# Performance work log

Hardware: AMD Instinct MI355X
Metric: run time of the kernel (lower is better)

Reference implementation:

```python
import jax, jax.numpy as jnp
import numpy as np

V = 100000   # nodes
E = 1600000  # edges (avg degree 16)
LN = 64      # feat_dim
S = 8        # stat_dim
T = 4        # recurrence steps
MU = 0.9
N_EDGE_TYPES = 10


def _uniform_linear(kw, kb, fan_out, fan_in):
    # torch nn.Linear default init: U(-1/sqrt(fan_in), 1/sqrt(fan_in))
    lim = 1.0 / np.sqrt(fan_in)
    W = jax.random.uniform(kw, (fan_out, fan_in), jnp.float32, -lim, lim)
    b = jax.random.uniform(kb, (fan_out,), jnp.float32, -lim, lim)
    return W, b


def setup_inputs() -> dict:
    key = jax.random.key(0)
    ks = jax.random.split(key, 12)
    feat_Matrix = jax.random.normal(ks[0], (V, LN), jnp.float32)
    X_Node = jax.random.randint(ks[1], (E,), 1, V + 1, dtype=jnp.int64)   # 1-indexed
    X_Neis = jax.random.randint(ks[2], (E,), 1, V + 1, dtype=jnp.int64)   # 1-indexed
    edge_type_index = jax.random.randint(ks[3], (E,), 1, N_EDGE_TYPES + 1, dtype=jnp.int32)
    dg_list = jax.random.randint(ks[4], (E,), 1, 65).astype(jnp.float32)  # degrees >= 1
    H_init = jax.random.uniform(ks[5], (V, S), jnp.float32)  # torch.rand init of state
    W_xi, b_xi = _uniform_linear(ks[6], ks[7], S * S, 2 * LN + N_EDGE_TYPES)
    W_rou, b_rou = _uniform_linear(ks[8], ks[9], S, LN)
    W1, b1 = _uniform_linear(ks[10], ks[11], 1, S)
    return {
        "feat_Matrix": feat_Matrix, "X_Node": X_Node, "X_Neis": X_Neis,
        "edge_type_index": edge_type_index, "dg_list": dg_list, "H_init": H_init,
        "W_xi": W_xi, "b_xi": b_xi, "W_rou": W_rou, "b_rou": b_rou,
        "W1": W1, "b1": b1,
    }


def reference(feat_Matrix, X_Node, X_Neis, edge_type_index, dg_list, H_init,
              W_xi, b_xi, W_rou, b_rou, W1, b1):
    src = X_Node - 1           # 0-indexed source nodes
    dst = X_Neis - 1           # 0-indexed neighbor nodes (for embedding gather)
    node_emb = feat_Matrix[src]            # [E, LN]
    neis_emb = feat_Matrix[dst]            # [E, LN]
    et = jax.nn.one_hot(edge_type_index - 1, N_EDGE_TYPES, dtype=jnp.float32)
    X = jnp.concatenate([node_emb, neis_emb, et], axis=1)  # [E, 2*LN+10]

    # Xi(X): per-edge transition matrices A, constant across steps -> precompute
    A = jnp.tanh(X @ W_xi.T + b_xi).reshape(-1, S, S)
    A = A * (MU / S) / dg_list[:, None, None]              # [E, S, S]
    # Rou(neis_emb): per-edge bias b, constant across steps
    bias = jnp.tanh(neis_emb @ W_rou.T + b_rou)            # [E, S]

    def step(H, _):
        He = H[src]                                        # gather [E, S]
        out = jnp.einsum('eij,ej->ei', A, He) + bias       # per-edge small matmul
        # AggrSum: dense one-hot mask vs RAW 1-indexed X_Neis against range(0,V-1)
        # -> scatter by 1-indexed ids; ids == V fall out of range and are dropped.
        Hn = jax.ops.segment_sum(out, X_Neis, num_segments=V)
        return Hn, None

    H, _ = jax.lax.scan(step, H_init, None, length=T)      # [V, S]

    logits = (H @ W1.T + b1).squeeze(-1)                   # [V]
    attn = jax.nn.softmax(logits)                          # softmax over nodes
    graph_out = jnp.tanh(jnp.sum(H * attn[:, None], axis=0))  # [S]
    return graph_out
```

## Files before the change

### kernel.cpp

```cpp
#include <hip/hip_runtime.h>
#include <hip/hip_bf16.h>

constexpr int V   = 100000;
constexpr int E   = 1600000;
constexpr int NET = 10;
constexpr int KXW = 138;
constexpr int NB  = (V + 255) / 256;
constexpr int GN  = 8;
constexpr float MUS   = 0.1125f;
constexpr float SP    = 0.025f;
constexpr float LOG2E = 1.44269504f;
constexpr float S2L   = 2.0f * SP * LOG2E;
constexpr float AS    = MUS / 127.0f;

typedef __attribute__((ext_vector_type(8))) short short8;
typedef __attribute__((ext_vector_type(4))) float float4v;

__device__ __forceinline__ float fast_tanh(float x) {
    return 1.0f - 2.0f * __builtin_amdgcn_rcpf(__expf(2.0f * x) + 1.0f);
}
__device__ __forceinline__ float bflo(unsigned u) { return __uint_as_float(u << 16); }
__device__ __forceinline__ float bfhi(unsigned u) { return __uint_as_float(u & 0xffff0000u); }
__device__ __forceinline__ short f2bf(float x) {
    union { __hip_bfloat16 b; short s; } u; u.b = __float2bfloat16(x); return u.s;
}

__device__ __forceinline__ float ub0(unsigned u) {
#if __has_builtin(__builtin_amdgcn_cvt_f32_ubyte0)
    return __builtin_amdgcn_cvt_f32_ubyte0(u);
#else
    return (float)(u & 0xff);
#endif
}
__device__ __forceinline__ float ub1(unsigned u) {
#if __has_builtin(__builtin_amdgcn_cvt_f32_ubyte1)
    return __builtin_amdgcn_cvt_f32_ubyte1(u);
#else
    return (float)((u >> 8) & 0xff);
#endif
}
__device__ __forceinline__ float ub2(unsigned u) {
#if __has_builtin(__builtin_amdgcn_cvt_f32_ubyte2)
    return __builtin_amdgcn_cvt_f32_ubyte2(u);
#else
    return (float)((u >> 16) & 0xff);
#endif
}
__device__ __forceinline__ float ub3(unsigned u) {
#if __has_builtin(__builtin_amdgcn_cvt_f32_ubyte3)
    return __builtin_amdgcn_cvt_f32_ubyte3(u);
#else
    return (float)(u >> 24);
#endif
}
__device__ __forceinline__ unsigned pku8(float f, unsigned pos, unsigned old) {
#if __has_builtin(__builtin_amdgcn_cvt_pk_u8_f32)
    return __builtin_amdgcn_cvt_pk_u8_f32(f, pos, old);
#else
    return old | ((unsigned)f << (8 * pos));
#endif
}

__device__ __forceinline__ int dot4(unsigned a, unsigned b, int c) {
#if __has_builtin(__builtin_amdgcn_sdot4)
    return __builtin_amdgcn_sdot4((int)a, (int)b, c, false);
#else
    int r = c;
    r += ((int)(a << 24) >> 24) * ((int)(b << 24) >> 24);
    r += ((int)(a << 16) >> 24) * ((int)(b << 16) >> 24);
    r += ((int)(a <<  8) >> 24) * ((int)(b <<  8) >> 24);
    r += ((int)a >> 24) * ((int)b >> 24);
    return r;
#endif
}

__global__ __launch_bounds__(256) void histg_kernel(
    const int* __restrict__ xneis, int* __restrict__ countg,
    int* __restrict__ rank0)
{
    int e = blockIdx.x * 256 + threadIdx.x;
    if (e >= E) return;
    int g = blockIdx.x & (GN - 1);
    int nr = xneis[e];
    if (nr < V) rank0[e] = atomicAdd(&countg[g * V + nr], 1);
}

__global__ __launch_bounds__(256) void gprefix_kernel(
    const int* __restrict__ countg, int* __restrict__ offg,
    int* __restrict__ cnt)
{
    int v = blockIdx.x * 256 + threadIdx.x;
    if (v >= V) return;
    int run = 0;
    #pragma unroll
    for (int g = 0; g < GN; ++g) {
        offg[g * V + v] = run;
        run += countg[g * V + v];
    }
    cnt[v] = run;
}

__global__ __launch_bounds__(256) void scan_cnt_kernel(
    const int* __restrict__ cnt, int* __restrict__ scanned, int* __restrict__ bsum)
{
    __shared__ int s[256];
    int tid = threadIdx.x;
    int i = blockIdx.x * 256 + tid;
    int c = (i < V) ? cnt[i] : 0;
    s[tid] = c; __syncthreads();
    #pragma unroll
    for (int off = 1; off < 256; off <<= 1) {
        int t = (tid >= off) ? s[tid - off] : 0;
        __syncthreads();
        s[tid] += t;
        __syncthreads();
    }
    if (i < V) scanned[i] = s[tid] - c;
    if (tid == 255) bsum[blockIdx.x] = s[255];
}

__global__ __launch_bounds__(512) void scan_tops_kernel(
    const int* __restrict__ blocksum, int* __restrict__ tops, int* __restrict__ rowptr)
{
    __shared__ int s[512];
    int tid = threadIdx.x;
    int v = (tid < NB) ? blocksum[tid] : 0;
    s[tid] = v; __syncthreads();
    #pragma unroll
    for (int off = 1; off < 512; off <<= 1) {
        int t = (tid >= off) ? s[tid - off] : 0;
        __syncthreads();
        s[tid] += t;
        __syncthreads();
    }
    if (tid < NB) tops[tid] = s[tid] - v;
    if (tid == 511) rowptr[V] = s[511];
}

__global__ __launch_bounds__(256) void add_offsets_kernel(
    const int* __restrict__ scanned, const int* __restrict__ tops, int* __restrict__ rowptr)
{
    int i = blockIdx.x * 256 + threadIdx.x;
    if (i < V) rowptr[i] = scanned[i] + tops[blockIdx.x];
}

__global__ __launch_bounds__(256) void scatter_kernel(
    const int* __restrict__ xnode, const int* __restrict__ xneis,
    const int* __restrict__ etype, const float* __restrict__ dg,
    const int* __restrict__ rowptr, const int* __restrict__ offg,
    const int* __restrict__ rank0, unsigned* __restrict__ pmeta)
{
    int e = blockIdx.x * 256 + threadIdx.x;
    if (e >= E) return;
    int g = blockIdx.x & (GN - 1);
    int nr = xneis[e];
    if (nr < V) {
        int p = rowptr[nr] + offg[g * V + nr] + rank0[e];
        unsigned src = (unsigned)(xnode[e] - 1);
        unsigned et  = (unsigned)(etype[e] - 1);
        unsigned dgi = (unsigned)dg[e] - 1;
        pmeta[p] = src | (et << 17) | (dgi << 21);
    }
}

__global__ __launch_bounds__(256) void bsum_kernel(
    const float* __restrict__ feat, const int* __restrict__ count,
    const float* __restrict__ Wrou, const float* __restrict__ brou,
    const float* __restrict__ Hinit, float* __restrict__ Bsum,
    uint4* __restrict__ Hq0)
{
    __shared__ float Wl[512];
    __shared__ float bl[8];
    int tid = threadIdx.x;
    for (int i = tid; i < 512; i += 256) Wl[i] = Wrou[i];
    if (tid < 8) bl[tid] = brou[tid];
    __syncthreads();

    int v = blockIdx.x * 256 + tid;
    if (v >= V) return;
    int c = count[v];
    float out[8] = {0, 0, 0, 0, 0, 0, 0, 0};
    if (c > 0) {
        const float4* f4 = (const float4*)(feat + (size_t)(v - 1) * 64);
        float acc[8];
        #pragma unroll
        for (int s = 0; s < 8; ++s) acc[s] = bl[s];
        #pragma unroll 4
        for (int k = 0; k < 16; ++k) {
            float4 x = f4[k];
            #pragma unroll
            for (int s = 0; s < 8; ++s) {
                const float* w = &Wl[s * 64 + k * 4];
                acc[s] += x.x * w[0] + x.y * w[1] + x.z * w[2] + x.w * w[3];
            }
        }
        float fc = (float)c;
        #pragma unroll
        for (int s = 0; s < 8; ++s) out[s] = fc * fast_tanh(acc[s]);
    }
    float4* O = (float4*)(Bsum + (size_t)v * 8);
    O[0] = make_float4(out[0], out[1], out[2], out[3]);
    O[1] = make_float4(out[4], out[5], out[6], out[7]);

    const float4* Hh4 = (const float4*)(Hinit + (size_t)v * 8);
    float4 h0 = Hh4[0], h1 = Hh4[1];
    float hv[8] = {h0.x, h0.y, h0.z, h0.w, h1.x, h1.y, h1.z, h1.w};
    float mx = 0.0f;
    #pragma unroll
    for (int i = 0; i < 8; ++i) mx = fmaxf(mx, fabsf(hv[i]));
    float si = (mx > 0.0f) ? 127.0f / mx : 0.0f;
    unsigned bb[8];
    #pragma unroll
    for (int i = 0; i < 8; ++i) bb[i] = (unsigned)((int)rintf(hv[i] * si)) & 0xffu;
    uint4 o;
    o.x = bb[0] | (bb[1] << 8) | (bb[2] << 16) | (bb[3] << 24);
    o.y = bb[4] | (bb[5] << 8) | (bb[6] << 16) | (bb[7] << 24);
    o.z = __float_as_uint(mx * (1.0f / 127.0f));
    o.w = 0;
    Hq0[v] = o;
}

__global__ __launch_bounds__(256) void pq_kernel(
    const float* __restrict__ feat, const float* __restrict__ Wxi,
    unsigned char* __restrict__ P8, ushort* __restrict__ Qb)
{
    const int lane = threadIdx.x & 63, wave = threadIdx.x >> 6;
    const int quad = lane >> 4, l16 = lane & 15;

    short8 bP[4][2], bQ[4][2];
    #pragma unroll
    for (int nt = 0; nt < 4; ++nt) {
        #pragma unroll
        for (int ks = 0; ks < 2; ++ks) {
            const float* wp = Wxi + (size_t)(nt * 16 + l16) * KXW + ks * 32 + quad * 8;
            short8 p, q;
            #pragma unroll
            for (int j = 0; j < 8; ++j) { p[j] = f2bf(wp[j]); q[j] = f2bf(wp[64 + j]); }
            bP[nt][ks] = p; bQ[nt][ks] = q;
        }
    }

    int t = blockIdx.x * 4 + wave;
    if (t >= V / 16) return;
    int v0 = t * 16;

    const float* fp = feat + (size_t)(v0 + l16) * 64 + quad * 8;
    short8 a0, a1;
    #pragma unroll
    for (int j = 0; j < 8; ++j) { a0[j] = f2bf(fp[j]); a1[j] = f2bf(fp[32 + j]); }

    float4v accP[4], accQ[4];
    #pragma unroll
    for (int nt = 0; nt < 4; ++nt) {
        float4v z = {0.f, 0.f, 0.f, 0.f};
        z = __builtin_amdgcn_mfma_f32_16x16x32_bf16(a0, bP[nt][0], z, 0, 0, 0);
        z = __builtin_amdgcn_mfma_f32_16x16x32_bf16(a1, bP[nt][1], z, 0, 0, 0);
        accP[nt] = z;
        float4v w = {0.f, 0.f, 0.f, 0.f};
        w = __builtin_amdgcn_mfma_f32_16x16x32_bf16(a0, bQ[nt][0], w, 0, 0, 0);
        w = __builtin_amdgcn_mfma_f32_16x16x32_bf16(a1, bQ[nt][1], w, 0, 0, 0);
        accQ[nt] = w;
    }

    #pragma unroll
    for (int r = 0; r < 4; ++r) {
        int row = v0 + quad * 4 + r;
        #pragma unroll
        for (int nt = 0; nt < 4; ++nt) {
            int col = nt * 16 + l16;
            int q8 = (int)rintf(accP[nt][r] * (1.0f / SP)) + 128;
            q8 = min(max(q8, 0), 255);
            P8[row * 64 + col] = (unsigned char)q8;
            Qb[row * 64 + col] = (ushort)f2bf(accQ[nt][r]);
        }
    }
}

__global__ __launch_bounds__(256) void amat_kernel(
    const unsigned* __restrict__ pmeta, const int* __restrict__ rowptr,
    const unsigned char* __restrict__ P8, const ushort* __restrict__ Qb,
    const float* __restrict__ Wxi, const float* __restrict__ bxi,
    const uint4* __restrict__ Hq0, const float* __restrict__ Bsum,
    unsigned char* __restrict__ A8, uint4* __restrict__ HqOut)
{
    __shared__ float Wet2[NET * 64];
    __shared__ float scT[64];
    int tid = threadIdx.x;
    for (int i = tid; i < NET * 64; i += 256) {
        int et = i >> 6, n = i & 63;
        Wet2[i] = 2.0f * LOG2E * (Wxi[n * KXW + 128 + et] + bxi[n]);
    }
    if (tid < 64) scT[tid] = 127.0f / (float)(tid + 1);
    __syncthreads();

    int v = blockIdx.x * 4 + (tid >> 6);
    if (v >= V) return;
    int lane = tid & 63;
    int el = lane >> 3, s = lane & 7;

    const int off = rowptr[v];
    const int deg = rowptr[v + 1] - off;

    float q0, q1, q2, q3, q4, q5, q6, q7;
    {
        uint4 qu = *(const uint4*)(Qb + v * 64 + s * 8);
        const float B = 128.0f * SP, C = 2.0f * LOG2E;
        q0 = C * (bflo(qu.x) - B); q1 = C * (bfhi(qu.x) - B);
        q2 = C * (bflo(qu.y) - B); q3 = C * (bfhi(qu.y) - B);
        q4 = C * (bflo(qu.z) - B); q5 = C * (bfhi(qu.z) - B);
        q6 = C * (bflo(qu.w) - B); q7 = C * (bfhi(qu.w) - B);
    }

    float accD = 0.0f;

    for (int base = 0; base < deg; base += 64) {
        unsigned m_mine = 0;
        {
            int i1 = base + lane;
            if (i1 < deg) m_mine = pmeta[off + i1];
        }
        int nb = deg - base;
        for (int k = 0; k * 8 + el < nb && k < 8; ++k) {
            int ib = k * 8 + el;
            int i = base + ib;
            unsigned m = __shfl(m_mine, ib);
            int src = (int)(m & 0x1FFFF);
            int et  = (int)((m >> 17) & 0xF);
            float kk  = scT[m >> 21];
            float m2k = -2.0f * kk;
            float ck  = kk + 128.5f;

            uint2 pu = *(const uint2*)(P8 + src * 64 + s * 8);
            const float4* w4 = (const float4*)(&Wet2[et * 64 + s * 8]);
            float4 wa = w4[0], wb = w4[1];
            uint4 hq = Hq0[src];

            float r0 = __builtin_amdgcn_rcpf(__builtin_amdgcn_exp2f(fmaf(ub0(pu.x), S2L, q0 + wa.x)) + 1.0f);
            float r1 = __builtin_amdgcn_rcpf(__builtin_amdgcn_exp2f(fmaf(ub1(pu.x), S2L, q1 + wa.y)) + 1.0f);
            float r2 = __builtin_amdgcn_rcpf(__builtin_amdgcn_exp2f(fmaf(ub2(pu.x), S2L, q2 + wa.z)) + 1.0f);
            float r3 = __builtin_amdgcn_rcpf(__builtin_amdgcn_exp2f(fmaf(ub3(pu.x), S2L, q3 + wa.w)) + 1.0f);
            float r4 = __builtin_amdgcn_rcpf(__builtin_amdgcn_exp2f(fmaf(ub0(pu.y), S2L, q4 + wb.x)) + 1.0f);
            float r5 = __builtin_amdgcn_rcpf(__builtin_amdgcn_exp2f(fmaf(ub1(pu.y), S2L, q5 + wb.y)) + 1.0f);
            float r6 = __builtin_amdgcn_rcpf(__builtin_amdgcn_exp2f(fmaf(ub2(pu.y), S2L, q6 + wb.z)) + 1.0f);
            float r7 = __builtin_amdgcn_rcpf(__builtin_amdgcn_exp2f(fmaf(ub3(pu.y), S2L, q7 + wb.w)) + 1.0f);

            float qf0 = fmaf(r0, m2k, ck), qf1 = fmaf(r1, m2k, ck);
            float qf2 = fmaf(r2, m2k, ck), qf3 = fmaf(r3, m2k, ck);
            float qf4 = fmaf(r4, m2k, ck), qf5 = fmaf(r5, m2k, ck);
            float qf6 = fmaf(r6, m2k, ck), qf7 = fmaf(r7, m2k, ck);

            uint2 o;
            o.x = pku8(qf3, 3, pku8(qf2, 2, pku8(qf1, 1, pku8(qf0, 0, 0u)))) ^ 0x80808080u;
            o.y = pku8(qf7, 3, pku8(qf6, 2, pku8(qf5, 1, pku8(qf4, 0, 0u)))) ^ 0x80808080u;
            *(uint2*)(A8 + (unsigned)(off + i) * 64u + (unsigned)(s * 8)) = o;

            int dd = dot4(o.x, hq.x, dot4(o.y, hq.y, 0));
            accD = fmaf((float)dd, __uint_as_float(hq.z), accD);
        }
    }
    accD += __shfl_xor(accD, 8);  accD += __shfl_xor(accD, 16); accD += __shfl_xor(accD, 32);
    float h1v = accD * AS + Bsum[v * 8 + s];

    float mx = fabsf(h1v);
    mx = fmaxf(mx, __shfl_xor(mx, 1));
    mx = fmaxf(mx, __shfl_xor(mx, 2));
    mx = fmaxf(mx, __shfl_xor(mx, 4));
    float si = (mx > 0.0f) ? 127.0f / mx : 0.0f;
    unsigned b = (unsigned)((int)rintf(h1v * si)) & 0xffu;
    unsigned b1 = __shfl(b, lane + 1), b2 = __shfl(b, lane + 2), b3 = __shfl(b, lane + 3);
    unsigned b4 = __shfl(b, lane + 4), b5 = __shfl(b, lane + 5);
    unsigned b6 = __shfl(b, lane + 6), b7 = __shfl(b, lane + 7);
    if (lane == 0) {
        uint4 hq;
        hq.x = b  | (b1 << 8) | (b2 << 16) | (b3 << 24);
        hq.y = b4 | (b5 << 8) | (b6 << 16) | (b7 << 24);
        hq.z = __float_as_uint(mx * (1.0f / 127.0f));
        hq.w = 0;
        HqOut[v] = hq;
    }
}

__global__ __launch_bounds__(256) void step_kernel(
    const uint4* __restrict__ HqIn, uint4* __restrict__ HqOut,
    const unsigned* __restrict__ pmeta, const int* __restrict__ rowptr,
    const unsigned char* __restrict__ A8, const float* __restrict__ Bsum,
    const float* __restrict__ W1, const float* __restrict__ b1,
    float* __restrict__ logitsOut, float* __restrict__ HfpOut)
{
    int v = blockIdx.x * 4 + (threadIdx.x >> 6);
    if (v >= V) return;
    int lane = threadIdx.x & 63;
    int el = lane >> 2, q = lane & 3;

    int p0 = rowptr[v], p1 = rowptr[v + 1];

    float accE = 0.0f, accO = 0.0f;
    int p = p0 + el;
    for (; p + 16 < p1; p += 32) {
        int srcA = (int)(pmeta[p] & 0x1FFFFu);
        int srcB = (int)(pmeta[p + 16] & 0x1FFFFu);
        uint4 auA = *(const uint4*)(A8 + (unsigned)p * 64u + (unsigned)(q * 16));
        uint4 auB = *(const uint4*)(A8 + (unsigned)(p + 16) * 64u + (unsigned)(q * 16));
        uint4 hqA = HqIn[srcA];
        uint4 hqB = HqIn[srcB];

        int dEA = dot4(auA.x, hqA.x, dot4(auA.y, hqA.y, 0));
        int dOA = dot4(auA.z, hqA.x, dot4(auA.w, hqA.y, 0));
        float sA = __uint_as_float(hqA.z);
        accE = fmaf((float)dEA, sA, accE);
        accO = fmaf((float)dOA, sA, accO);

        int dEB = dot4(auB.x, hqB.x, dot4(auB.y, hqB.y, 0));
        int dOB = dot4(auB.z, hqB.x, dot4(auB.w, hqB.y, 0));
        float sB = __uint_as_float(hqB.z);
        accE = fmaf((float)dEB, sB, accE);
        accO = fmaf((float)dOB, sB, accO);
    }
    if (p < p1) {
        int src = (int)(pmeta[p] & 0x1FFFFu);
        uint4 au = *(const uint4*)(A8 + (unsigned)p * 64u + (unsigned)(q * 16));
        uint4 hq = HqIn[src];
        int dE = dot4(au.x, hq.x, dot4(au.y, hq.y, 0));
        int dO = dot4(au.z, hq.x, dot4(au.w, hq.y, 0));
        float sc = __uint_as_float(hq.z);
        accE = fmaf((float)dE, sc, accE);
        accO = fmaf((float)dO, sc, accO);
    }
    accE += __shfl_xor(accE, 4);  accE += __shfl_xor(accE, 8);
    accE += __shfl_xor(accE, 16); accE += __shfl_xor(accE, 32);
    accO += __shfl_xor(accO, 4);  accO += __shfl_xor(accO, 8);
    accO += __shfl_xor(accO, 16); accO += __shfl_xor(accO, 32);

    float hE = accE * AS + Bsum[v * 8 + q * 2];
    float hO = accO * AS + Bsum[v * 8 + q * 2 + 1];

    float mx = fmaxf(fabsf(hE), fabsf(hO));
    mx = fmaxf(mx, __shfl_xor(mx, 1));
    mx = fmaxf(mx, __shfl_xor(mx, 2));
    float si = (mx > 0.0f) ? 127.0f / mx : 0.0f;
    unsigned qE = (unsigned)((int)rintf(hE * si)) & 0xffu;
    unsigned qO = (unsigned)((int)rintf(hO * si)) & 0xffu;
    unsigned hw  = qE | (qO << 8);
    unsigned hw1 = __shfl(hw, lane + 1), hw2 = __shfl(hw, lane + 2);
    unsigned hw3 = __shfl(hw, lane + 3);
    if (lane == 0) {
        uint4 o;
        o.x = hw  | (hw1 << 16);
        o.y = hw2 | (hw3 << 16);
        o.z = __float_as_uint(mx * (1.0f / 127.0f));
        o.w = 0;
        HqOut[v] = o;
    }
    if (HfpOut != nullptr && el == 0)
        *(float2*)(HfpOut + v * 8 + q * 2) = make_float2(hE, hO);
    if (logitsOut != nullptr) {
        float t = hE * W1[q * 2] + hO * W1[q * 2 + 1];
        t += __shfl_xor(t, 1); t += __shfl_xor(t, 2);
        if (lane == 0) logitsOut[v] = t + b1[0];
    }
}

__global__ __launch_bounds__(256) void reduce_max_kernel(
    const float* __restrict__ logits, float* __restrict__ partial)
{
    float m = -INFINITY;
    for (int v = blockIdx.x * 256 + threadIdx.x; v < V; v += 256 * 256)
        m = fmaxf(m, logits[v]);
    #pragma unroll
    for (int o = 32; o > 0; o >>= 1) m = fmaxf(m, __shfl_down(m, o));
    __shared__ float sm[4];
    if ((threadIdx.x & 63) == 0) sm[threadIdx.x >> 6] = m;
    __syncthreads();
    if (threadIdx.x == 0)
        partial[blockIdx.x] = fmaxf(fmaxf(sm[0], sm[1]), fmaxf(sm[2], sm[3]));
}

__global__ __launch_bounds__(256) void final_max_kernel(
    const float* __restrict__ partial, float* __restrict__ M)
{
    float m = partial[threadIdx.x];
    #pragma unroll
    for (int o = 32; o > 0; o >>= 1) m = fmaxf(m, __shfl_down(m, o));
    __shared__ float sm[4];
    if ((threadIdx.x & 63) == 0) sm[threadIdx.x >> 6] = m;
    __syncthreads();
    if (threadIdx.x == 0) *M = fmaxf(fmaxf(sm[0], sm[1]), fmaxf(sm[2], sm[3]));
}

__global__ __launch_bounds__(256) void sum_kernel(
    const float* __restrict__ H, const float* __restrict__ logits,
    const float* __restrict__ Mp, float* __restrict__ partial)
{
    const float M = *Mp;
    float se = 0.0f;
    float sh[8] = {0, 0, 0, 0, 0, 0, 0, 0};
    for (int v = blockIdx.x * 256 + threadIdx.x; v < V; v += 64 * 256) {
        float w = __expf(logits[v] - M);
        se += w;
        const float4* H4 = (const float4*)(H + (size_t)v * 8);
        float4 h0 = H4[0], h1 = H4[1];
        sh[0] += w * h0.x; sh[1] += w * h0.y; sh[2] += w * h0.z; sh[3] += w * h0.w;
        sh[4] += w * h1.x; sh[5] += w * h1.y; sh[6] += w * h1.z; sh[7] += w * h1.w;
    }
    #pragma unroll
    for (int o = 32; o > 0; o >>= 1) {
        se += __shfl_xor(se, o);
        #pragma unroll
        for (int i = 0; i < 8; ++i) sh[i] += __shfl_xor(sh[i], o);
    }
    __shared__ float sm[4][9];
    int wv = threadIdx.x >> 6;
    if ((threadIdx.x & 63) == 0) {
        sm[wv][8] = se;
        #pragma unroll
        for (int i = 0; i < 8; ++i) sm[wv][i] = sh[i];
    }
    __syncthreads();
    if (threadIdx.x == 0) {
        #pragma unroll
        for (int i = 0; i < 9; ++i)
            partial[blockIdx.x * 12 + i] = sm[0][i] + sm[1][i] + sm[2][i] + sm[3][i];
    }
}

__global__ void final_kernel(const float* __restrict__ partial, float* __restrict__ out)
{
    int lane = threadIdx.x;
    float vals[9];
    #pragma unroll
    for (int i = 0; i < 9; ++i) vals[i] = partial[lane * 12 + i];
    #pragma unroll
    for (int o = 1; o < 64; o <<= 1) {
        #pragma unroll
        for (int i = 0; i < 9; ++i) vals[i] += __shfl_xor(vals[i], o);
    }
    __shared__ float res[9];
    if (lane == 0) {
        #pragma unroll
        for (int i = 0; i < 9; ++i) res[i] = vals[i];
    }
    __syncthreads();
    if (lane < 8) out[lane] = tanhf(res[lane] / res[8]);
}

extern "C" void kernel_launch(void* const* d_in, const int* in_sizes, int n_in,
                              void* d_out, int out_size, void* d_ws, size_t ws_size,
                              hipStream_t stream)
{
    const float* feat  = (const float*)d_in[0];
    const int*   xnode = (const int*)d_in[1];
    const int*   xneis = (const int*)d_in[2];
    const int*   etype = (const int*)d_in[3];
    const float* dg    = (const float*)d_in[4];
    const float* Hinit = (const float*)d_in[5];
    const float* Wxi   = (const float*)d_in[6];
    const float* bxi   = (const float*)d_in[7];
    const float* Wrou  = (const float*)d_in[8];
    const float* brou  = (const float*)d_in[9];
    const float* W1    = (const float*)d_in[10];
    const float* b1    = (const float*)d_in[11];

    char* ws = (char*)d_ws;
    auto alloc = [&](size_t bytes) -> char* {
        char* p = ws; ws += (bytes + 255) & ~(size_t)255; return p;
    };
    unsigned char* A8 = (unsigned char*)alloc((size_t)E * 64);
    unsigned char* P8 = (unsigned char*)alloc((size_t)V * 64);
    ushort*   Qb      = (ushort*)alloc((size_t)V * 64 * 2);
    unsigned* pmeta   = (unsigned*)alloc((size_t)E * 4);
    int*      rank0   = (int*)alloc((size_t)E * 4);
    int*      countg  = (int*)alloc((size_t)GN * V * 4);
    int*      offg    = (int*)alloc((size_t)GN * V * 4);
    int*      cnt     = (int*)alloc((size_t)V * 4);
    int*      scanned = (int*)alloc((size_t)V * 4);
    int*      rowptr  = (int*)alloc((size_t)(V + 1) * 4);
    int*      bsumT   = (int*)alloc(512 * 4);
    int*      topsT   = (int*)alloc(512 * 4);
    uint4*    Hq0     = (uint4*)alloc((size_t)V * 16);
    uint4*    HqA     = (uint4*)alloc((size_t)V * 16);
    uint4*    HqB     = (uint4*)alloc((size_t)V * 16);
    float*    Hfp     = (float*)alloc((size_t)V * 8 * 4);
    float*    Bsum    = (float*)alloc((size_t)V * 8 * 4);
    float*    logits  = (float*)alloc((size_t)V * 4);
    float*    pmax    = (float*)alloc(256 * 4);
    float*    Mp      = (float*)alloc(16);
    float*    spart   = (float*)alloc(64 * 12 * 4);

    hipMemsetAsync(countg, 0, (size_t)GN * V * 4, stream);
    histg_kernel<<<(E + 255) / 256, 256, 0, stream>>>(xneis, countg, rank0);
    gprefix_kernel<<<NB, 256, 0, stream>>>(countg, offg, cnt);
    scan_cnt_kernel<<<NB, 256, 0, stream>>>(cnt, scanned, bsumT);
    scan_tops_kernel<<<1, 512, 0, stream>>>(bsumT, topsT, rowptr);
    add_offsets_kernel<<<NB, 256, 0, stream>>>(scanned, topsT, rowptr);
    scatter_kernel<<<(E + 255) / 256, 256, 0, stream>>>(xnode, xneis, etype, dg,
                                                        rowptr, offg, rank0, pmeta);
    pq_kernel<<<(V / 16 + 3) / 4, 256, 0, stream>>>(feat, Wxi, P8, Qb);
    bsum_kernel<<<NB, 256, 0, stream>>>(feat, cnt, Wrou, brou, Hinit,
                                        Bsum, Hq0);
    amat_kernel<<<(V + 3) / 4, 256, 0, stream>>>(pmeta, rowptr, P8, Qb, Wxi, bxi,
                                                 Hq0, Bsum, A8, HqA);

    const uint4* Hcur = HqA;
    uint4* bufs[2] = {HqB, HqA};
    for (int t = 0; t < 3; ++t) {
        uint4* Hn = bufs[t & 1];
        float* lg  = (t == 2) ? logits : nullptr;
        float* hf  = (t == 2) ? Hfp : nullptr;
        step_kernel<<<(V + 3) / 4, 256, 0, stream>>>(Hcur, Hn, pmeta, rowptr,
                                                     A8, Bsum, W1, b1, lg, hf);
        Hcur = Hn;
    }

    reduce_max_kernel<<<256, 256, 0, stream>>>(logits, pmax);
    final_max_kernel<<<1, 256, 0, stream>>>(pmax, Mp);
    sum_kernel<<<64, 256, 0, stream>>>(Hfp, logits, Mp, spart);
    final_kernel<<<1, 64, 0, stream>>>(spart, (float*)d_out);
}
```

Before: 454.5 us.

## Map four lanes per node in step kernel and fuse prefix kernels

The step kernel now assigns four lanes per destination node, so a wavefront handles 16 nodes instead of one, and each lane walks the node's edges serially. This drops the cross-lane shuffle reductions and the idle lanes seen with low-degree nodes (average 16 edges, and only 16 of 64 lanes were used per pass). The risk is less memory-level parallelism per node and load imbalance across lanes when node degrees differ. Separately, the group-prefix kernel is fused into the count scan kernel, which removes one launch and one round trip through the count array.

```diff
diff --git a/kernel.cpp b/kernel.cpp
--- a/kernel.cpp
+++ b/kernel.cpp
@@ -85,28 +85,24 @@
     if (nr < V) rank0[e] = atomicAdd(&countg[g * V + nr], 1);
 }
 
-__global__ __launch_bounds__(256) void gprefix_kernel(
+__global__ __launch_bounds__(256) void scanV_kernel(
     const int* __restrict__ countg, int* __restrict__ offg,
-    int* __restrict__ cnt)
-{
-    int v = blockIdx.x * 256 + threadIdx.x;
-    if (v >= V) return;
-    int run = 0;
-    #pragma unroll
-    for (int g = 0; g < GN; ++g) {
-        offg[g * V + v] = run;
-        run += countg[g * V + v];
-    }
-    cnt[v] = run;
-}
-
-__global__ __launch_bounds__(256) void scan_cnt_kernel(
-    const int* __restrict__ cnt, int* __restrict__ scanned, int* __restrict__ bsum)
+    int* __restrict__ cnt_tot, int* __restrict__ scanned, int* __restrict__ bsum)
 {
     __shared__ int s[256];
     int tid = threadIdx.x;
     int i = blockIdx.x * 256 + tid;
-    int c = (i < V) ? cnt[i] : 0;
+    int c = 0;
+    if (i < V) {
+        int run = 0;
+        #pragma unroll
+        for (int g = 0; g < GN; ++g) {
+            offg[g * V + i] = run;
+            run += countg[g * V + i];
+        }
+        cnt_tot[i] = run;
+        c = run;
+    }
     s[tid] = c; __syncthreads();
     #pragma unroll
     for (int off = 1; off < 256; off <<= 1) {
@@ -387,37 +383,16 @@
     const float* __restrict__ W1, const float* __restrict__ b1,
     float* __restrict__ logitsOut, float* __restrict__ HfpOut)
 {
-    int v = blockIdx.x * 4 + (threadIdx.x >> 6);
+    int v = blockIdx.x * 64 + (threadIdx.x >> 2);
     if (v >= V) return;
-    int lane = threadIdx.x & 63;
-    int el = lane >> 2, q = lane & 3;
+    int q = threadIdx.x & 3;
 
     int p0 = rowptr[v], p1 = rowptr[v + 1];
 
     float accE = 0.0f, accO = 0.0f;
-    int p = p0 + el;
-    for (; p + 16 < p1; p += 32) {
-        int srcA = (int)(pmeta[p] & 0x1FFFFu);
-        int srcB = (int)(pmeta[p + 16] & 0x1FFFFu);
-        uint4 auA = *(const uint4*)(A8 + (unsigned)p * 64u + (unsigned)(q * 16));
-        uint4 auB = *(const uint4*)(A8 + (unsigned)(p + 16) * 64u + (unsigned)(q * 16));
-        uint4 hqA = HqIn[srcA];
-        uint4 hqB = HqIn[srcB];
-
-        int dEA = dot4(auA.x, hqA.x, dot4(auA.y, hqA.y, 0));
-        int dOA = dot4(auA.z, hqA.x, dot4(auA.w, hqA.y, 0));
-        float sA = __uint_as_float(hqA.z);
-        accE = fmaf((float)dEA, sA, accE);
-        accO = fmaf((float)dOA, sA, accO);
-
-        int dEB = dot4(auB.x, hqB.x, dot4(auB.y, hqB.y, 0));
-        int dOB = dot4(auB.z, hqB.x, dot4(auB.w, hqB.y, 0));
-        float sB = __uint_as_float(hqB.z);
-        accE = fmaf((float)dEB, sB, accE);
-        accO = fmaf((float)dOB, sB, accO);
-    }
-    if (p < p1) {
-        int src = (int)(pmeta[p] & 0x1FFFFu);
+    for (int p = p0; p < p1; ++p) {
+        unsigned m = pmeta[p];
+        int src = (int)(m & 0x1FFFFu);
         uint4 au = *(const uint4*)(A8 + (unsigned)p * 64u + (unsigned)(q * 16));
         uint4 hq = HqIn[src];
         int dE = dot4(au.x, hq.x, dot4(au.y, hq.y, 0));
@@ -426,10 +401,6 @@
         accE = fmaf((float)dE, sc, accE);
         accO = fmaf((float)dO, sc, accO);
     }
-    accE += __shfl_xor(accE, 4);  accE += __shfl_xor(accE, 8);
-    accE += __shfl_xor(accE, 16); accE += __shfl_xor(accE, 32);
-    accO += __shfl_xor(accO, 4);  accO += __shfl_xor(accO, 8);
-    accO += __shfl_xor(accO, 16); accO += __shfl_xor(accO, 32);
 
     float hE = accE * AS + Bsum[v * 8 + q * 2];
     float hO = accO * AS + Bsum[v * 8 + q * 2 + 1];
@@ -440,23 +411,23 @@
     float si = (mx > 0.0f) ? 127.0f / mx : 0.0f;
     unsigned qE = (unsigned)((int)rintf(hE * si)) & 0xffu;
     unsigned qO = (unsigned)((int)rintf(hO * si)) & 0xffu;
-    unsigned hw  = qE | (qO << 8);
-    unsigned hw1 = __shfl(hw, lane + 1), hw2 = __shfl(hw, lane + 2);
-    unsigned hw3 = __shfl(hw, lane + 3);
-    if (lane == 0) {
+    unsigned hw = qE | (qO << 8);
+    unsigned w0 = hw | (__shfl_xor(hw, 1) << 16);
+    unsigned w1 = __shfl_xor(w0, 2);
+    if (q == 0) {
         uint4 o;
-        o.x = hw  | (hw1 << 16);
-        o.y = hw2 | (hw3 << 16);
+        o.x = w0;
+        o.y = w1;
         o.z = __float_as_uint(mx * (1.0f / 127.0f));
         o.w = 0;
         HqOut[v] = o;
     }
-    if (HfpOut != nullptr && el == 0)
+    if (HfpOut != nullptr)
         *(float2*)(HfpOut + v * 8 + q * 2) = make_float2(hE, hO);
     if (logitsOut != nullptr) {
         float t = hE * W1[q * 2] + hO * W1[q * 2 + 1];
         t += __shfl_xor(t, 1); t += __shfl_xor(t, 2);
-        if (lane == 0) logitsOut[v] = t + b1[0];
+        if (q == 0) logitsOut[v] = t + b1[0];
     }
 }
 
@@ -588,8 +559,7 @@
 
     hipMemsetAsync(countg, 0, (size_t)GN * V * 4, stream);
     histg_kernel<<<(E + 255) / 256, 256, 0, stream>>>(xneis, countg, rank0);
-    gprefix_kernel<<<NB, 256, 0, stream>>>(countg, offg, cnt);
-    scan_cnt_kernel<<<NB, 256, 0, stream>>>(cnt, scanned, bsumT);
+    scanV_kernel<<<NB, 256, 0, stream>>>(countg, offg, cnt, scanned, bsumT);
     scan_tops_kernel<<<1, 512, 0, stream>>>(bsumT, topsT, rowptr);
     add_offsets_kernel<<<NB, 256, 0, stream>>>(scanned, topsT, rowptr);
     scatter_kernel<<<(E + 255) / 256, 256, 0, stream>>>(xnode, xneis, etype, dg,
@@ -606,8 +576,8 @@
         uint4* Hn = bufs[t & 1];
         float* lg  = (t == 2) ? logits : nullptr;
         float* hf  = (t == 2) ? Hfp : nullptr;
-        step_kernel<<<(V + 3) / 4, 256, 0, stream>>>(Hcur, Hn, pmeta, rowptr,
-                                                     A8, Bsum, W1, b1, lg, hf);
+        step_kernel<<<(V + 63) / 64, 256, 0, stream>>>(Hcur, Hn, pmeta, rowptr,
+                                                       A8, Bsum, W1, b1, lg, hf);
         Hcur = Hn;
     }
 
```

Result: no change. 459.4 us (+1.1%).
